# Optimization experiments

Measured on AMD Instinct MI355X. Metric: run time of the kernel, lower is better.

## Reference

```python
import jax, jax.numpy as jnp
import numpy as np

ODE_DIM = 512
BATCH = 32768
N_STEPS = 50  # (T - t0) / dt with dt = (1-0)/(50*n_layers), n_layers=1
DT = 1.0 / N_STEPS


def setup_inputs() -> dict:
    key = jax.random.key(0)
    k_x, k_w, k_b, k_g = jax.random.split(key, 4)
    x = jax.random.normal(k_x, (BATCH, ODE_DIM), dtype=jnp.float32)
    # nn.Linear(ODE_dim, ODE_dim) default init ~ U(-1/sqrt(d), 1/sqrt(d))
    bound = 1.0 / np.sqrt(ODE_DIM)
    W_in = jax.random.uniform(k_w, (ODE_DIM, ODE_DIM), dtype=jnp.float32,
                              minval=-bound, maxval=bound)
    b_in = jax.random.uniform(k_b, (ODE_DIM,), dtype=jnp.float32,
                              minval=-bound, maxval=bound)
    # gamma_layer = bias of an nn.Linear(ODE_dim, ODE_dim)
    gamma = jax.random.uniform(k_g, (ODE_DIM,), dtype=jnp.float32,
                               minval=-bound, maxval=bound)
    return {"x": x, "W_in": W_in, "b_in": b_in, "gamma": gamma}


def reference(x, W_in, b_in, gamma):
    # architecture = 'inside_weights' (-1):
    #   rhs(x) = x @ diag(gamma) + tanh(x @ W_in^T + b_in)
    # diag(gamma) on the right is a per-column elementwise scale.
    def euler_step(state, _):
        rhs = state * gamma + jnp.tanh(state @ W_in.T + b_in)
        return state + DT * rhs, None

    out, _ = jax.lax.scan(euler_step, x, None, length=N_STEPS)
    return out
```

## Files before the change

kernel.cpp:

```cpp
#include <hip/hip_runtime.h>
#include <cstdint>
#include <cstddef>


#define D_DIM 512
#define NSTEPS 50
#define A_STRIDE 520

typedef __bf16 bf16x8 __attribute__((ext_vector_type(8)));
typedef float f32x4 __attribute__((ext_vector_type(4)));
typedef unsigned short ushort8_t __attribute__((ext_vector_type(8)));

__device__ __forceinline__ unsigned short f_to_bf16_bits(float f) {
    union { float f; unsigned int i; } c;
    c.f = f;
    unsigned int u = c.i;
    unsigned int r = (u + 0x7fffu + ((u >> 16) & 1u)) >> 16;
    return (unsigned short)r;
}

__global__ __launch_bounds__(256) void build_wl(
    const float* __restrict__ W, unsigned short* __restrict__ Wl) {
    int f = blockIdx.x * 256 + threadIdx.x;
    int quad = f & 3;
    int l16  = (f >> 2) & 15;
    int t    = (f >> 6) & 3;
    int kb   = (f >> 8) & 15;
    int w    = f >> 12;
    int i    = t * 16 + l16;
    int srow = w * 64 + 4 * (i & 15) + (i >> 4);
    int k0   = kb * 32 + quad * 8;
    float4 a = *(const float4*)&W[(size_t)srow * D_DIM + k0];
    float4 b = *(const float4*)&W[(size_t)srow * D_DIM + k0 + 4];
    ushort8_t o;
    o[0] = f_to_bf16_bits(a.x); o[1] = f_to_bf16_bits(a.y);
    o[2] = f_to_bf16_bits(a.z); o[3] = f_to_bf16_bits(a.w);
    o[4] = f_to_bf16_bits(b.x); o[5] = f_to_bf16_bits(b.y);
    o[6] = f_to_bf16_bits(b.z); o[7] = f_to_bf16_bits(b.w);
    *(ushort8_t*)&Wl[(size_t)f * 8] = o;
}

__global__ __launch_bounds__(512, 2) void node_persist(
    const float* __restrict__ X,
    const unsigned short* __restrict__ Wl,
    const float* __restrict__ bias,
    const float* __restrict__ gamma,
    float* __restrict__ Fout)
{
    __shared__ unsigned short ldsA[2][64 * A_STRIDE];

    const int tid  = threadIdx.x;
    const int lane = tid & 63;
    const int w    = tid >> 6;
    const int l16  = lane & 15;
    const int quad = lane >> 4;
    const int bm   = blockIdx.x;
    const float dt = 1.0f / 50.0f;

    const int ctrue0 = w * 64 + 4 * l16;

    const unsigned short* bpw =
        Wl + (size_t)w * 32768 + (size_t)(l16 * 4 + quad) * 8;

    float bc_[4], g1_[4];
    {
        float4 b4 = *(const float4*)&bias[ctrue0];
        float4 g4 = *(const float4*)&gamma[ctrue0];
        bc_[0] = b4.x; bc_[1] = b4.y; bc_[2] = b4.z; bc_[3] = b4.w;
        g1_[0] = 1.0f + dt * g4.x; g1_[1] = 1.0f + dt * g4.y;
        g1_[2] = 1.0f + dt * g4.z; g1_[3] = 1.0f + dt * g4.w;
    }

    const int r0 = quad * 4;
    float s[4][4][4];
#pragma unroll
    for (int tm = 0; tm < 4; ++tm)
#pragma unroll
        for (int r = 0; r < 4; ++r) {
            float4 v = *(const float4*)
                &X[(size_t)(bm * 64 + r0 + tm * 16 + r) * D_DIM + ctrue0];
            s[tm][0][r] = v.x; s[tm][1][r] = v.y;
            s[tm][2][r] = v.z; s[tm][3][r] = v.w;
        }

#pragma unroll
    for (int tm = 0; tm < 4; ++tm)
#pragma unroll
        for (int r = 0; r < 4; ++r) {
            ushort4 h;
            h.x = f_to_bf16_bits(s[tm][0][r]);
            h.y = f_to_bf16_bits(s[tm][1][r]);
            h.z = f_to_bf16_bits(s[tm][2][r]);
            h.w = f_to_bf16_bits(s[tm][3][r]);
            *(ushort4*)&ldsA[0][(r0 + tm * 16 + r) * A_STRIDE + ctrue0] = h;
        }

    bf16x8 bfp[4][4];
#pragma unroll
    for (int pj = 0; pj < 4; ++pj)
#pragma unroll
        for (int t = 0; t < 4; ++t)
            bfp[pj][t] = *reinterpret_cast<const bf16x8*>(
                bpw + (12 + pj) * 2048 + t * 512);

    bf16x8 bf0[4], bf1[4];
#pragma unroll
    for (int t = 0; t < 4; ++t)
        bf0[t] = *reinterpret_cast<const bf16x8*>(bpw + t * 512);

    __syncthreads();

#define LDB(bf, kb) do {                                                   \
    _Pragma("unroll")                                                      \
    for (int t_ = 0; t_ < 4; ++t_)                                         \
        bf[t_] = *reinterpret_cast<const bf16x8*>(                         \
            bpw + (kb) * 2048 + t_ * 512);                                 \
} while (0)

#define LDA(af, buf, kb) do {                                              \
    _Pragma("unroll")                                                      \
    for (int tm_ = 0; tm_ < 4; ++tm_)                                      \
        af[tm_] = *reinterpret_cast<const bf16x8*>(                        \
            &ldsA[buf][(tm_ * 16 + l16) * A_STRIDE + (kb) * 32 + quad * 8]); \
} while (0)

#define MFMA16(af, bf) do {                                                \
    _Pragma("unroll")                                                      \
    for (int tm_ = 0; tm_ < 4; ++tm_)                                      \
        _Pragma("unroll")                                                  \
        for (int tn_ = 0; tn_ < 4; ++tn_)                                  \
            acc[tm_][tn_] = __builtin_amdgcn_mfma_f32_16x16x32_bf16(       \
                af[tm_], bf[tn_], acc[tm_][tn_], 0, 0, 0);                 \
} while (0)

    int p = 0;
    for (int step = 0; step < NSTEPS; ++step) {
        f32x4 acc[4][4];
#pragma unroll
        for (int tm = 0; tm < 4; ++tm)
#pragma unroll
            for (int tn = 0; tn < 4; ++tn) {
                f32x4 b4 = {bc_[tn], bc_[tn], bc_[tn], bc_[tn]};
                acc[tm][tn] = b4;
            }

        bf16x8 af[4];
#pragma unroll
        for (int j = 0; j < 6; ++j) {
            const int kb = 2 * j;
            LDB(bf1, kb + 1);
            LDA(af, p, kb);
            MFMA16(af, bf0);
            if (j < 4) {
                LDA(af, p, 12 + j);
                MFMA16(af, bfp[j]);
            }
            LDB(bf0, (kb + 2) % 12);
            LDA(af, p, kb + 1);
            MFMA16(af, bf1);
        }

#pragma unroll
        for (int tm = 0; tm < 4; ++tm)
#pragma unroll
            for (int tn = 0; tn < 4; ++tn)
#pragma unroll
                for (int r = 0; r < 4; ++r) {
                    float y = acc[tm][tn][r];
                    float e = __expf(2.0f * y);
                    float th = 1.0f - 2.0f * __builtin_amdgcn_rcpf(e + 1.0f);
                    s[tm][tn][r] = s[tm][tn][r] * g1_[tn] + dt * th;
                }

        if (step == NSTEPS - 1) break;

#pragma unroll
        for (int tm = 0; tm < 4; ++tm)
#pragma unroll
            for (int r = 0; r < 4; ++r) {
                ushort4 h;
                h.x = f_to_bf16_bits(s[tm][0][r]);
                h.y = f_to_bf16_bits(s[tm][1][r]);
                h.z = f_to_bf16_bits(s[tm][2][r]);
                h.w = f_to_bf16_bits(s[tm][3][r]);
                *(ushort4*)&ldsA[p ^ 1][(r0 + tm * 16 + r) * A_STRIDE + ctrue0] = h;
            }
        __syncthreads();
        p ^= 1;
    }

#pragma unroll
    for (int tm = 0; tm < 4; ++tm)
#pragma unroll
        for (int r = 0; r < 4; ++r) {
            float4 v;
            v.x = s[tm][0][r]; v.y = s[tm][1][r];
            v.z = s[tm][2][r]; v.w = s[tm][3][r];
            *(float4*)&Fout[(size_t)(bm * 64 + r0 + tm * 16 + r) * D_DIM + ctrue0] = v;
        }
}

extern "C" void kernel_launch(void* const* d_in, const int* in_sizes, int n_in,
                              void* d_out, int out_size, void* d_ws, size_t ws_size,
                              hipStream_t stream) {
    const float* x  = (const float*)d_in[0];
    const float* W  = (const float*)d_in[1];
    const float* bi = (const float*)d_in[2];
    const float* ga = (const float*)d_in[3];

    unsigned short* Wl = (unsigned short*)d_ws;

    build_wl<<<128, 256, 0, stream>>>(W, Wl);
    node_persist<<<dim3(512), dim3(512), 0, stream>>>(
        x, Wl, bi, ga, (float*)d_out);
}
```

Before: 1.631 ms.

## Stream weight tiles into LDS via async global_load_lds with double buffering

Weight fragments were previously loaded from global memory straight into registers, with 4 k-blocks kept resident. They are now staged into a per-wave double-buffered LDS area using global_load_lds, and each k-block is then read back from LDS. To make room, the state buffer in LDS drops from double to single buffering, which adds a __syncthreads before each state write-back. The intent is to free registers and hide weight-load latency, at the cost of extra LDS traffic, an added barrier per step, and a hand-tuned vmcnt wait that assumes no wave reads LDS data another wave writes.

```diff
diff --git a/kernel.cpp b/kernel.cpp
--- a/kernel.cpp
+++ b/kernel.cpp
@@ -21,12 +21,13 @@
 
 __global__ __launch_bounds__(256) void build_wl(
     const float* __restrict__ W, unsigned short* __restrict__ Wl) {
-    int f = blockIdx.x * 256 + threadIdx.x;
-    int quad = f & 3;
-    int l16  = (f >> 2) & 15;
+    int f    = blockIdx.x * 256 + threadIdx.x;
+    int lane = f & 63;
     int t    = (f >> 6) & 3;
     int kb   = (f >> 8) & 15;
     int w    = f >> 12;
+    int l16  = lane & 15;
+    int quad = lane >> 4;
     int i    = t * 16 + l16;
     int srow = w * 64 + 4 * (i & 15) + (i >> 4);
     int k0   = kb * 32 + quad * 8;
@@ -47,7 +48,8 @@
     const float* __restrict__ gamma,
     float* __restrict__ Fout)
 {
-    __shared__ unsigned short ldsA[2][64 * A_STRIDE];
+    __shared__ unsigned short ldsA[64 * A_STRIDE];
+    __shared__ unsigned short ldsB[2][8][4][64 * 8];
 
     const int tid  = threadIdx.x;
     const int lane = tid & 63;
@@ -59,8 +61,7 @@
 
     const int ctrue0 = w * 64 + 4 * l16;
 
-    const unsigned short* bpw =
-        Wl + (size_t)w * 32768 + (size_t)(l16 * 4 + quad) * 8;
+    const unsigned short* bpw = Wl + (size_t)w * 32768 + (size_t)lane * 8;
 
     float bc_[4], g1_[4];
     {
@@ -92,48 +93,25 @@
             h.y = f_to_bf16_bits(s[tm][1][r]);
             h.z = f_to_bf16_bits(s[tm][2][r]);
             h.w = f_to_bf16_bits(s[tm][3][r]);
-            *(ushort4*)&ldsA[0][(r0 + tm * 16 + r) * A_STRIDE + ctrue0] = h;
-        }
-
-    bf16x8 bfp[4][4];
-#pragma unroll
-    for (int pj = 0; pj < 4; ++pj)
-#pragma unroll
-        for (int t = 0; t < 4; ++t)
-            bfp[pj][t] = *reinterpret_cast<const bf16x8*>(
-                bpw + (12 + pj) * 2048 + t * 512);
-
-    bf16x8 bf0[4], bf1[4];
-#pragma unroll
-    for (int t = 0; t < 4; ++t)
-        bf0[t] = *reinterpret_cast<const bf16x8*>(bpw + t * 512);
+            *(ushort4*)&ldsA[(r0 + tm * 16 + r) * A_STRIDE + ctrue0] = h;
+        }
+
+#define STAGE(kb_) do {                                                      \
+    const int b_ = (kb_) & 1, s_ = (kb_) & 15;                               \
+    _Pragma("unroll")                                                        \
+    for (int t_ = 0; t_ < 4; ++t_)                                           \
+        __builtin_amdgcn_global_load_lds(                                    \
+            (const __attribute__((address_space(1))) unsigned int*)          \
+                (bpw + (size_t)s_ * 2048 + t_ * 512),                        \
+            (__attribute__((address_space(3))) unsigned int*)                \
+                &ldsB[b_][w][t_][0],                                         \
+            16, 0, 0);                                                       \
+} while (0)
+
+    STAGE(0);
 
     __syncthreads();
 
-#define LDB(bf, kb) do {                                                   \
-    _Pragma("unroll")                                                      \
-    for (int t_ = 0; t_ < 4; ++t_)                                         \
-        bf[t_] = *reinterpret_cast<const bf16x8*>(                         \
-            bpw + (kb) * 2048 + t_ * 512);                                 \
-} while (0)
-
-#define LDA(af, buf, kb) do {                                              \
-    _Pragma("unroll")                                                      \
-    for (int tm_ = 0; tm_ < 4; ++tm_)                                      \
-        af[tm_] = *reinterpret_cast<const bf16x8*>(                        \
-            &ldsA[buf][(tm_ * 16 + l16) * A_STRIDE + (kb) * 32 + quad * 8]); \
-} while (0)
-
-#define MFMA16(af, bf) do {                                                \
-    _Pragma("unroll")                                                      \
-    for (int tm_ = 0; tm_ < 4; ++tm_)                                      \
-        _Pragma("unroll")                                                  \
-        for (int tn_ = 0; tn_ < 4; ++tn_)                                  \
-            acc[tm_][tn_] = __builtin_amdgcn_mfma_f32_16x16x32_bf16(       \
-                af[tm_], bf[tn_], acc[tm_][tn_], 0, 0, 0);                 \
-} while (0)
-
-    int p = 0;
     for (int step = 0; step < NSTEPS; ++step) {
         f32x4 acc[4][4];
 #pragma unroll
@@ -144,20 +122,26 @@
                 acc[tm][tn] = b4;
             }
 
-        bf16x8 af[4];
-#pragma unroll
-        for (int j = 0; j < 6; ++j) {
-            const int kb = 2 * j;
-            LDB(bf1, kb + 1);
-            LDA(af, p, kb);
-            MFMA16(af, bf0);
-            if (j < 4) {
-                LDA(af, p, 12 + j);
-                MFMA16(af, bfp[j]);
+#pragma unroll
+        for (int kb = 0; kb < 16; ++kb) {
+            STAGE(kb + 1);
+            asm volatile("s_waitcnt vmcnt(4)" ::: "memory");
+            __builtin_amdgcn_sched_barrier(0);
+            const int b = kb & 1;
+            bf16x8 af[4], bf[4];
+#pragma unroll
+            for (int t = 0; t < 4; ++t) {
+                af[t] = *reinterpret_cast<const bf16x8*>(
+                    &ldsA[(t * 16 + l16) * A_STRIDE + kb * 32 + quad * 8]);
+                bf[t] = *reinterpret_cast<const bf16x8*>(
+                    &ldsB[b][w][t][lane * 8]);
             }
-            LDB(bf0, (kb + 2) % 12);
-            LDA(af, p, kb + 1);
-            MFMA16(af, bf1);
+#pragma unroll
+            for (int tm = 0; tm < 4; ++tm)
+#pragma unroll
+                for (int tn = 0; tn < 4; ++tn)
+                    acc[tm][tn] = __builtin_amdgcn_mfma_f32_16x16x32_bf16(
+                        af[tm], bf[tn], acc[tm][tn], 0, 0, 0);
         }
 
 #pragma unroll
@@ -174,6 +158,7 @@
 
         if (step == NSTEPS - 1) break;
 
+        __syncthreads();
 #pragma unroll
         for (int tm = 0; tm < 4; ++tm)
 #pragma unroll
@@ -183,10 +168,9 @@
                 h.y = f_to_bf16_bits(s[tm][1][r]);
                 h.z = f_to_bf16_bits(s[tm][2][r]);
                 h.w = f_to_bf16_bits(s[tm][3][r]);
-                *(ushort4*)&ldsA[p ^ 1][(r0 + tm * 16 + r) * A_STRIDE + ctrue0] = h;
+                *(ushort4*)&ldsA[(r0 + tm * 16 + r) * A_STRIDE + ctrue0] = h;
             }
         __syncthreads();
-        p ^= 1;
     }
 
 #pragma unroll
```

After: 1.768 ms. 1.08x slower.
